# Kernel tuning notes

Measured on AMD Instinct MI355X. Metric: run time of the kernel, lower is better.

## Reference

```python
import jax, jax.numpy as jnp
import numpy as np

B, S, D, H = 2, 2048, 1024, 16
HD = D // H  # head_dim = 64


def setup_inputs() -> dict:
    key = jax.random.key(0)
    ks = jax.random.split(key, 9)
    scale = 0.02
    x = jax.random.normal(ks[0], (B, S, D), dtype=jnp.float32)
    wq = jax.random.normal(ks[1], (D, D), dtype=jnp.float32) * scale
    bq = jnp.zeros((D,), dtype=jnp.float32)
    wk = jax.random.normal(ks[2], (D, D), dtype=jnp.float32) * scale
    bk = jnp.zeros((D,), dtype=jnp.float32)
    wv = jax.random.normal(ks[3], (D, D), dtype=jnp.float32) * scale
    bv = jnp.zeros((D,), dtype=jnp.float32)
    wo = jax.random.normal(ks[4], (D, D), dtype=jnp.float32) * scale
    bo = jnp.zeros((D,), dtype=jnp.float32)
    # causal mask: 1.0 where key position is in the future of query position
    mask = jnp.triu(jnp.ones((S, S), dtype=jnp.float32), k=1)[None, None]  # [1,1,S,S]
    return {"x": x, "wq": wq, "bq": bq, "wk": wk, "bk": bk,
            "wv": wv, "bv": bv, "wo": wo, "bo": bo, "mask": mask}


def reference(x, wq, bq, wk, bk, wv, bv, wo, bo, mask):
    b, s, d = x.shape
    q = (x @ wq + bq).reshape(b, s, H, HD).transpose(0, 2, 1, 3)  # [b,h,s,hd]
    k = (x @ wk + bk).reshape(b, s, H, HD).transpose(0, 2, 1, 3)
    v = (x @ wv + bv).reshape(b, s, H, HD).transpose(0, 2, 1, 3)
    scores = jnp.einsum('bhqd,bhkd->bhqk', q, k) / jnp.sqrt(jnp.float32(HD))
    scores = scores + mask * (-1e9)
    probs = jax.nn.softmax(scores, axis=-1)
    out = jnp.einsum('bhqk,bhkd->bhqd', probs, v)
    out = out.transpose(0, 2, 1, 3).reshape(b, s, d)
    return out @ wo + bo
```

## Files before the change

### kernel.cpp

```cpp
#include <hip/hip_runtime.h>
#include <hip/hip_bf16.h>
#include <cstdint>

#define DEV static __device__ __forceinline__

typedef unsigned short u16t;
typedef __attribute__((ext_vector_type(4))) float f32x4;
typedef __attribute__((ext_vector_type(4))) unsigned short u16x4;
typedef __attribute__((ext_vector_type(8))) unsigned short u16x8;
typedef __attribute__((ext_vector_type(8))) __bf16 bf16x8;

DEV u16t f2bf(float f) {
  unsigned u = __builtin_bit_cast(unsigned, f);
  u += 0x7fffu + ((u >> 16) & 1u);
  return (u16t)(u >> 16);
}
DEV float bf2f(u16t h) {
  unsigned u = ((unsigned)h) << 16;
  return __builtin_bit_cast(float, u);
}

DEV void gload_lds16(const void* g, void* l) {
  __builtin_amdgcn_global_load_lds(
      (const __attribute__((address_space(1))) void*)g,
      (__attribute__((address_space(3))) void*)l, 16, 0, 0);
}

DEV bf16x8 ldsfrag(const u16t* p) {
  return __builtin_bit_cast(bf16x8, *(const u16x8*)p);
}

DEV void bsync() {
  asm volatile("" ::: "memory");
  __builtin_amdgcn_s_barrier();
  asm volatile("" ::: "memory");
}

__global__ __launch_bounds__(256) void k_convert_x(const float* __restrict__ x,
                                                   u16t* __restrict__ xb) {
  int i = (blockIdx.x * 256 + threadIdx.x) * 4;
  f32x4 v = *(const f32x4*)&x[i];
  u16x4 o;
#pragma unroll
  for (int j = 0; j < 4; ++j) o[j] = f2bf(v[j]);
  *(u16x4*)&xb[i] = o;
}

__global__ __launch_bounds__(256) void k_transw(const float* __restrict__ w0,
                                                const float* __restrict__ w1,
                                                const float* __restrict__ w2,
                                                const float* __restrict__ w3,
                                                u16t* __restrict__ qkvT,
                                                u16t* __restrict__ oT) {
  __shared__ float lds[64][68];
  int z = blockIdx.z;
  const float* W = (z == 0) ? w0 : (z == 1) ? w1 : (z == 2) ? w2 : w3;
  u16t* OUT = (z < 3) ? (qkvT + (size_t)z * 1024 * 1024) : oT;
  int k0 = blockIdx.x * 64, n0 = blockIdx.y * 64;
  int t = threadIdx.x;
  int kl = t >> 4, n4 = (t & 15) << 2;
#pragma unroll
  for (int p = 0; p < 4; ++p) {
    f32x4 v = *(const f32x4*)&W[(size_t)(k0 + kl + p * 16) * 1024 + n0 + n4];
    *(f32x4*)&lds[kl + p * 16][n4] = v;
  }
  __syncthreads();
  int nl = t >> 4, k4 = (t & 15) << 2;
#pragma unroll
  for (int p = 0; p < 4; ++p) {
    int n = nl + p * 16;
    u16x4 o;
#pragma unroll
    for (int i = 0; i < 4; ++i) o[i] = f2bf(lds[k4 + i][n]);
    *(u16x4*)&OUT[(size_t)(n0 + n) * 1024 + k0 + k4] = o;
  }
}

template <bool BF16_OUT, bool VSPLIT>
__global__ __launch_bounds__(256) void k_gemm_bt(const u16t* __restrict__ A,
                                                 const u16t* __restrict__ BT,
                                                 void* __restrict__ Cout,
                                                 const float* __restrict__ b0,
                                                 const float* __restrict__ b1,
                                                 const float* __restrict__ b2,
                                                 u16t* __restrict__ vt,
                                                 int M, int N, int K) {
  __shared__ u16t Al[2][128 * 64];
  __shared__ u16t Bl[2][128 * 64];
  const int tid = threadIdx.x;
  const int l = tid & 63;
  const int w = tid >> 6;
  const int m0 = blockIdx.x * 128, n0 = blockIdx.y * 128;
  const int wm = (w >> 1) * 64, wn = (w & 1) * 64;
  const int lm = l & 15, lh = l >> 4;
  f32x4 acc[4][4] = {};

  auto stage = [&](int bb, int t) {
    const int k0 = t << 6;
#pragma unroll
    for (int s = 0; s < 4; ++s) {
      int c = s * 256 + tid;
      int row = c >> 3, slot = c & 7;
      int ks = k0 + (((slot ^ (row & 7)) & 7) << 3);
      gload_lds16(A + (size_t)(m0 + row) * K + ks, &Al[bb][c * 8]);
    }
#pragma unroll
    for (int s = 0; s < 4; ++s) {
      int c = s * 256 + tid;
      int row = c >> 3, slot = c & 7;
      int ks = k0 + (((slot ^ (row & 7)) & 7) << 3);
      gload_lds16(BT + (size_t)(n0 + row) * K + ks, &Bl[bb][c * 8]);
    }
  };

  const int nt = K >> 6;
  stage(0, 0);
  for (int t = 0; t < nt; ++t) {
    if (t + 1 < nt) {
      stage((t + 1) & 1, t + 1);
      asm volatile("s_waitcnt vmcnt(8)" ::: "memory");
    } else {
      asm volatile("s_waitcnt vmcnt(0)" ::: "memory");
    }
    bsync();
    const int buf = t & 1;

#pragma unroll
    for (int kk = 0; kk < 2; ++kk) {
      bf16x8 af[4], bfr[4];
#pragma unroll
      for (int i = 0; i < 4; ++i) {
        int ra = wm + i * 16 + lm;
        int sa = (kk * 4 + lh) ^ (ra & 7);
        af[i] = ldsfrag(&Al[buf][ra * 64 + sa * 8]);
        int rb = wn + i * 16 + lm;
        int sb = (kk * 4 + lh) ^ (rb & 7);
        bfr[i] = ldsfrag(&Bl[buf][rb * 64 + sb * 8]);
      }
#pragma unroll
      for (int i = 0; i < 4; ++i)
#pragma unroll
        for (int j = 0; j < 4; ++j)
          acc[i][j] = __builtin_amdgcn_mfma_f32_16x16x32_bf16(af[i], bfr[j],
                                                              acc[i][j], 0, 0, 0);
    }
    bsync();
  }

  if (!VSPLIT || (n0 + wn) < 2048) {
#pragma unroll
    for (int i = 0; i < 4; ++i) {
      int row = m0 + wm + i * 16 + (lh << 2);
#pragma unroll
      for (int j = 0; j < 4; ++j) {
        int col = n0 + wn + j * 16 + lm;
        const float* bp = (col < 1024) ? b0 : ((col < 2048) ? b1 : b2);
        float bias = bp[col & 1023];
#pragma unroll
        for (int r = 0; r < 4; ++r) {
          float v = acc[i][j][r] + bias;
          if (BF16_OUT)
            ((u16t*)Cout)[(size_t)(row + r) * N + col] = f2bf(v);
          else
            ((float*)Cout)[(size_t)(row + r) * N + col] = v;
        }
      }
    }
  } else {
#pragma unroll
    for (int i = 0; i < 4; ++i) {
      int row = m0 + wm + i * 16 + (lh << 2);
      int bidx = row >> 11, s0 = row & 2047;
#pragma unroll
    for (int j = 0; j < 4; ++j) {
        int col = n0 + wn + j * 16 + lm;
        int d = col - 2048;
        int hh = d >> 6, dd = d & 63;
        float bias = b2[d];
        u16x4 o;
#pragma unroll
        for (int r = 0; r < 4; ++r) o[r] = f2bf(acc[i][j][r] + bias);
        *(u16x4*)&vt[((size_t)((bidx * 16 + hh) * 64 + dd)) * 2048 + s0] = o;
      }
    }
  }
}

__global__ __launch_bounds__(256, 4) void k_attn(const u16t* __restrict__ qkv,
                                                 const u16t* __restrict__ vt,
                                                 u16t* __restrict__ outp) {
  __shared__ u16t Kl[4096];
  __shared__ u16t Vl[4096];
  __shared__ u16t Pl[4][1024];
  const int tid = threadIdx.x, l = tid & 63, w = tid >> 6;
  const int lm = l & 15, lh = l >> 4;
  const int bh = blockIdx.x, b = bh >> 4, h = bh & 15;
  const int y = blockIdx.y;
  const int qt = (y < 8) ? y : (y < 16) ? (39 - y) : (y < 24) ? (y - 8) : (47 - y);
  const int q0 = qt * 64;
  const int nt = qt + 1;

  bf16x8 aq[2];
  const int qrow = q0 + w * 16 + lm;
#pragma unroll
  for (int kk = 0; kk < 2; ++kk) {
    const u16t* src = qkv + (size_t)(b * 2048 + qrow) * 3072 + h * 64 + kk * 32 + lh * 8;
    u16x8 v = *(const u16x8*)src;
    u16x8 o;
#pragma unroll
    for (int e = 0; e < 8; ++e) o[e] = f2bf(bf2f(v[e]) * 0.125f);
    aq[kk] = __builtin_bit_cast(bf16x8, o);
  }

  float mrun = -1e30f;
  float lsum = 0.f;
  f32x4 aco[4] = {};

  const u16t* Kg = qkv + (size_t)b * 2048 * 3072 + 1024 + h * 64;
  const u16t* Vg = vt + (size_t)bh * 64 * 2048;
  u16t* Pw = &Pl[w][0];

  auto stage = [&](int t) {
#pragma unroll
    for (int s = 0; s < 2; ++s) {
      int c = s * 256 + tid;
      int row = c >> 3, col = ((c & 7) ^ (row & 7)) << 3;
      gload_lds16(Kg + (size_t)(t * 64 + row) * 3072 + col, &Kl[c * 8]);
    }
#pragma unroll
    for (int s = 0; s < 2; ++s) {
      int c = s * 256 + tid;
      int row = c >> 3, col = ((c & 7) ^ (row & 7)) << 3;
      gload_lds16(Vg + (size_t)row * 2048 + t * 64 + col, &Vl[c * 8]);
    }
  };

  for (int t = 0; t < nt; ++t) {
    stage(t);
    asm volatile("s_waitcnt vmcnt(0)" ::: "memory");
    bsync();

    f32x4 accs[4] = {};
#pragma unroll
    for (int kk = 0; kk < 2; ++kk) {
      bf16x8 ak[4];
#pragma unroll
      for (int nk = 0; nk < 4; ++nk) {
        int rk = nk * 16 + lm;
        int s16 = (kk * 4 + lh) ^ (rk & 7);
        ak[nk] = ldsfrag(&Kl[rk * 64 + s16 * 8]);
      }
      __builtin_amdgcn_s_setprio(1);
#pragma unroll
      for (int nk = 0; nk < 4; ++nk)
        accs[nk] = __builtin_amdgcn_mfma_f32_16x16x32_bf16(ak[nk], aq[kk],
                                                           accs[nk], 0, 0, 0);
      __builtin_amdgcn_s_setprio(0);
    }

    float vmax = -1e30f;
    if (t == nt - 1) {
#pragma unroll
      for (int nk = 0; nk < 4; ++nk)
#pragma unroll
        for (int r = 0; r < 4; ++r) {
          int kvpos = t * 64 + nk * 16 + lh * 4 + r;
          float v = accs[nk][r];
          v = (kvpos > qrow) ? -1e30f : v;
          accs[nk][r] = v;
          vmax = fmaxf(vmax, v);
        }
    } else {
#pragma unroll
      for (int nk = 0; nk < 4; ++nk)
#pragma unroll
        for (int r = 0; r < 4; ++r) vmax = fmaxf(vmax, accs[nk][r]);
    }

    if (!__all(vmax <= mrun + 8.f)) {
      float rm = fmaxf(vmax, __shfl_xor(vmax, 16));
      rm = fmaxf(rm, __shfl_xor(rm, 32));
      float mnew = fmaxf(mrun, rm);
      float alpha = __expf(mrun - mnew);
      mrun = mnew;
      lsum *= alpha;
#pragma unroll
      for (int r = 0; r < 4; ++r) {
        float ar = __shfl(alpha, lh * 4 + r);
#pragma unroll
        for (int nd = 0; nd < 4; ++nd) aco[nd][r] *= ar;
      }
    }

#pragma unroll
    for (int nk = 0; nk < 4; ++nk) {
      u16x4 pb;
#pragma unroll
      for (int r = 0; r < 4; ++r) {
        float p = __expf(accs[nk][r] - mrun);
        lsum += p;
        pb[r] = f2bf(p);
      }
      int s16 = (nk * 2 + (lh >> 1)) ^ (lm & 7);
      *(u16x4*)&Pw[lm * 64 + s16 * 8 + (lh & 1) * 4] = pb;
    }

#pragma unroll
    for (int kk = 0; kk < 2; ++kk) {
      int s16p = (kk * 4 + lh) ^ (lm & 7);
      bf16x8 ap = ldsfrag(&Pw[lm * 64 + s16p * 8]);
      __builtin_amdgcn_s_setprio(1);
#pragma unroll
      for (int nd = 0; nd < 4; ++nd) {
        int rv = nd * 16 + lm;
        int s16v = (kk * 4 + lh) ^ (rv & 7);
        bf16x8 bv = ldsfrag(&Vl[rv * 64 + s16v * 8]);
        aco[nd] = __builtin_amdgcn_mfma_f32_16x16x32_bf16(ap, bv, aco[nd], 0, 0, 0);
      }
      __builtin_amdgcn_s_setprio(0);
    }

    bsync();
  }

  lsum += __shfl_xor(lsum, 16);
  lsum += __shfl_xor(lsum, 32);
  float inv = 1.0f / lsum;
#pragma unroll
  for (int r = 0; r < 4; ++r) {
    float ir = __shfl(inv, lh * 4 + r);
    int row = q0 + w * 16 + lh * 4 + r;
#pragma unroll
    for (int nd = 0; nd < 4; ++nd) {
      int col = h * 64 + nd * 16 + lm;
      outp[(size_t)(b * 2048 + row) * 1024 + col] = f2bf(aco[nd][r] * ir);
    }
  }
}

extern "C" void kernel_launch(void* const* d_in, const int* in_sizes, int n_in,
                              void* d_out, int out_size, void* d_ws, size_t ws_size,
                              hipStream_t stream) {
  const float* x = (const float*)d_in[0];
  const float* wq = (const float*)d_in[1];
  const float* bq = (const float*)d_in[2];
  const float* wk = (const float*)d_in[3];
  const float* bk = (const float*)d_in[4];
  const float* wv = (const float*)d_in[5];
  const float* bv = (const float*)d_in[6];
  const float* wo = (const float*)d_in[7];
  const float* bo = (const float*)d_in[8];

  char* ws = (char*)d_ws;
  u16t* xb = (u16t*)ws;
  u16t* wqkvT = (u16t*)(ws + (8u << 20));
  u16t* woT = (u16t*)(ws + (14u << 20));
  u16t* qkv = (u16t*)(ws + (16u << 20));
  u16t* vt = (u16t*)(ws + (40u << 20));
  u16t* attn_out = xb;

  k_convert_x<<<4096, 256, 0, stream>>>(x, xb);
  k_transw<<<dim3(16, 16, 4), 256, 0, stream>>>(wq, wk, wv, wo, wqkvT, woT);
  k_gemm_bt<true, true><<<dim3(32, 24), 256, 0, stream>>>(xb, wqkvT, qkv, bq, bk,
                                                          bv, vt, 4096, 3072, 1024);
  k_attn<<<dim3(32, 32), 256, 0, stream>>>(qkv, vt, attn_out);
  k_gemm_bt<false, false><<<dim3(32, 8), 256, 0, stream>>>(
      attn_out, woT, d_out, bo, bo, bo, nullptr, 4096, 1024, 1024);
}
```

Measured before the change: 112.3 us.

## Process two KV subtiles per barrier round and switch softmax to exp2

The attention loop now stages two 64-row K/V subtiles into double-sized LDS buffers before one wait and barrier, then computes both. This halves the barrier and wait rounds per query tile and keeps more global loads in flight. The second subtile is skipped when it lies entirely past the causal diagonal, although it is still loaded. Q is also prescaled by log2(e)/sqrt(d) so the softmax can use exp2f instead of __expf. The cost is doubled K/V LDS, about 40KB per block, which may limit occupancy, plus wasted loads on even query tiles.

```diff
diff --git a/kernel.cpp b/kernel.cpp
--- a/kernel.cpp
+++ b/kernel.cpp
@@ -189,8 +189,8 @@
 __global__ __launch_bounds__(256, 4) void k_attn(const u16t* __restrict__ qkv,
                                                  const u16t* __restrict__ vt,
                                                  u16t* __restrict__ outp) {
-  __shared__ u16t Kl[4096];
-  __shared__ u16t Vl[4096];
+  __shared__ u16t Kl[2][4096];
+  __shared__ u16t Vl[2][4096];
   __shared__ u16t Pl[4][1024];
   const int tid = threadIdx.x, l = tid & 63, w = tid >> 6;
   const int lm = l & 15, lh = l >> 4;
@@ -198,7 +198,7 @@
   const int y = blockIdx.y;
   const int qt = (y < 8) ? y : (y < 16) ? (39 - y) : (y < 24) ? (y - 8) : (47 - y);
   const int q0 = qt * 64;
-  const int nt = qt + 1;
+  const int nt = (qt >> 1) + 1;
 
   bf16x8 aq[2];
   const int qrow = q0 + w * 16 + lm;
@@ -208,7 +208,7 @@
     u16x8 v = *(const u16x8*)src;
     u16x8 o;
 #pragma unroll
-    for (int e = 0; e < 8; ++e) o[e] = f2bf(bf2f(v[e]) * 0.125f);
+    for (int e = 0; e < 8; ++e) o[e] = f2bf(bf2f(v[e]) * 0.1803368801f);
     aq[kk] = __builtin_bit_cast(bf16x8, o);
   }
 
@@ -220,26 +220,22 @@
   const u16t* Vg = vt + (size_t)bh * 64 * 2048;
   u16t* Pw = &Pl[w][0];
 
-  auto stage = [&](int t) {
+  auto stage = [&](int sub, int kv0) {
 #pragma unroll
     for (int s = 0; s < 2; ++s) {
       int c = s * 256 + tid;
       int row = c >> 3, col = ((c & 7) ^ (row & 7)) << 3;
-      gload_lds16(Kg + (size_t)(t * 64 + row) * 3072 + col, &Kl[c * 8]);
+      gload_lds16(Kg + (size_t)(kv0 + row) * 3072 + col, &Kl[sub][c * 8]);
     }
 #pragma unroll
     for (int s = 0; s < 2; ++s) {
       int c = s * 256 + tid;
       int row = c >> 3, col = ((c & 7) ^ (row & 7)) << 3;
-      gload_lds16(Vg + (size_t)row * 2048 + t * 64 + col, &Vl[c * 8]);
+      gload_lds16(Vg + (size_t)row * 2048 + kv0 + col, &Vl[sub][c * 8]);
     }
   };
 
-  for (int t = 0; t < nt; ++t) {
-    stage(t);
-    asm volatile("s_waitcnt vmcnt(0)" ::: "memory");
-    bsync();
-
+  auto subtile = [&](int sub, int kv0) {
     f32x4 accs[4] = {};
 #pragma unroll
     for (int kk = 0; kk < 2; ++kk) {
@@ -248,7 +244,7 @@
       for (int nk = 0; nk < 4; ++nk) {
         int rk = nk * 16 + lm;
         int s16 = (kk * 4 + lh) ^ (rk & 7);
-        ak[nk] = ldsfrag(&Kl[rk * 64 + s16 * 8]);
+        ak[nk] = ldsfrag(&Kl[sub][rk * 64 + s16 * 8]);
       }
       __builtin_amdgcn_s_setprio(1);
 #pragma unroll
@@ -259,12 +255,12 @@
     }
 
     float vmax = -1e30f;
-    if (t == nt - 1) {
+    if (kv0 + 63 > q0) {
 #pragma unroll
       for (int nk = 0; nk < 4; ++nk)
 #pragma unroll
         for (int r = 0; r < 4; ++r) {
-          int kvpos = t * 64 + nk * 16 + lh * 4 + r;
+          int kvpos = kv0 + nk * 16 + lh * 4 + r;
           float v = accs[nk][r];
           v = (kvpos > qrow) ? -1e30f : v;
           accs[nk][r] = v;
@@ -281,7 +277,7 @@
       float rm = fmaxf(vmax, __shfl_xor(vmax, 16));
       rm = fmaxf(rm, __shfl_xor(rm, 32));
       float mnew = fmaxf(mrun, rm);
-      float alpha = __expf(mrun - mnew);
+      float alpha = exp2f(mrun - mnew);
       mrun = mnew;
       lsum *= alpha;
 #pragma unroll
@@ -297,7 +293,7 @@
       u16x4 pb;
 #pragma unroll
       for (int r = 0; r < 4; ++r) {
-        float p = __expf(accs[nk][r] - mrun);
+        float p = exp2f(accs[nk][r] - mrun);
         lsum += p;
         pb[r] = f2bf(p);
       }
@@ -314,11 +310,22 @@
       for (int nd = 0; nd < 4; ++nd) {
         int rv = nd * 16 + lm;
         int s16v = (kk * 4 + lh) ^ (rv & 7);
-        bf16x8 bv = ldsfrag(&Vl[rv * 64 + s16v * 8]);
+        bf16x8 bv = ldsfrag(&Vl[sub][rv * 64 + s16v * 8]);
         aco[nd] = __builtin_amdgcn_mfma_f32_16x16x32_bf16(ap, bv, aco[nd], 0, 0, 0);
       }
       __builtin_amdgcn_s_setprio(0);
     }
+  };
+
+  for (int t = 0; t < nt; ++t) {
+    const int kvA = t * 128, kvB = kvA + 64;
+    stage(0, kvA);
+    stage(1, kvB);
+    asm volatile("s_waitcnt vmcnt(0)" ::: "memory");
+    bsync();
+
+    subtile(0, kvA);
+    if (kvB <= q0 + 63) subtile(1, kvB);
 
     bsync();
   }
```

Measured after the change: 114.2 us. No clear change (+1.7%).
